# Performance work log

Measured on AMD Instinct MI355X. Metric: run time of the kernel, lower is better.

The kernel has to match this reference:

```python
import jax, jax.numpy as jnp
import numpy as np

H, K, D, HID, B = 8, 2048, 64, 1024, 8192
TEMP = 1.0
LN_EPS = 1e-5


def setup_inputs() -> dict:
    key = jax.random.key(0)
    ks = jax.random.split(key, 6)
    s = lambda k, shape, scale=0.02: jax.random.normal(k, shape, jnp.float32) * scale
    return dict(
        z=jax.random.normal(ks[0], (B, HID), jnp.float32),
        w1=s(ks[1], (H, HID, 2 * D)),
        b1=jnp.zeros((H, 2 * D), jnp.float32),
        w2=s(ks[2], (H, 2 * D, D)),
        b2=jnp.zeros((H, D), jnp.float32),
        ln_g=jnp.ones((H, D), jnp.float32),
        ln_b=jnp.zeros((H, D), jnp.float32),
        codebooks=jax.random.normal(ks[3], (H, K, D), jnp.float32) * 0.1,
        dec_w=s(ks[4], (H, D, HID // H)),
        dec_b=jnp.zeros((H, HID // H), jnp.float32),
    )


def reference(z, w1, b1, w2, b2, ln_g, ln_b, codebooks, dec_w, dec_b):
    sg = jax.lax.stop_gradient
    Bf = z.shape[0]
    # per-head projection MLP (all heads fused via einsum): [B,HID] -> [B,H,2D] -> [B,H,D]
    h1 = jax.nn.gelu(jnp.einsum('bi,hio->bho', z, w1) + b1, approximate=False)
    zh = jnp.einsum('bho,hod->bhd', h1, w2) + b2
    mu = zh.mean(-1, keepdims=True)
    var = zh.var(-1, keepdims=True)  # biased, as torch LayerNorm
    z_heads = (zh - mu) / jnp.sqrt(var + LN_EPS) * ln_g + ln_b  # [B,H,D]
    # squared-distance to codebooks: ||z||^2 + ||c||^2 - 2 z.c  -> [B,H,K]
    z_sq = (z_heads ** 2).sum(-1)[..., None]          # [B,H,1]
    c_sq = (codebooks ** 2).sum(-1)[None]             # [1,H,K]
    zc = jnp.einsum('bhd,hkd->bhk', z_heads, codebooks)
    dists = z_sq + c_sq - 2.0 * zc
    idx = jnp.argmin(dists, axis=-1)                  # [B,H] int
    z_q = codebooks[jnp.arange(H)[None, :], idx]      # gather -> [B,H,D]
    # per-head decoders then concat -> [B,HID]
    dec = lambda x: (jnp.einsum('bhd,hdo->bho', x, dec_w) + dec_b).reshape(Bf, -1)
    z_q_dec = dec(z_q)
    z_proj = dec(z_heads)
    z_q_st = z_proj + sg(z_q_dec - z_proj)
    commit = jnp.mean((z_proj - sg(z_q_dec)) ** 2)
    codebook_loss = jnp.mean((sg(z_proj) - z_q_dec) ** 2)
    # entropy regularizer over soft assignment probs
    probs = jax.nn.softmax(-dists * TEMP, axis=-1)    # [B,H,K]
    avg_probs = probs.mean(0)                         # [H,K]
    entropy = -(avg_probs * jnp.log(avg_probs + 1e-8)).sum(-1).mean()
    entropy_loss = 1.0 - entropy / np.float32(np.log(K))
    # orthogonality: pairwise co-occurrence deviation from independence
    p = jnp.zeros((H, K), jnp.float32).at[jnp.arange(H)[None, :], idx].add(1.0) / Bf  # [H,K]
    ortho = jnp.float32(0.0)
    cnt = 0
    for i in range(H):
        for j in range(i + 1, H):
            co = jnp.zeros((K, K), jnp.float32).at[idx[:, i], idx[:, j]].add(1.0) / (Bf + 1e-8)
            expected = p[i][:, None] * p[j][None, :]
            ortho = ortho + jnp.mean(jnp.abs(co - expected))
            cnt += 1
    ortho = ortho / cnt
    return z_q_st, idx, commit, codebook_loss, entropy_loss, ortho, sg(z_heads)
```

## Files before the change

### kernel.cpp

```cpp
#include <hip/hip_runtime.h>
#include <math.h>

#define H 8
#define KK 2048
#define DD 64
#define HIDN 1024
#define BB 8192
#define TWO_D 128
#define OO 128

#define WS_CSQ   1048576
#define WS_ZSQ   1064960
#define WS_IDX   1130496
#define WS_AVGP  1196032
#define WS_HIST  1212416
#define WS_ACC   1228800
#define WS_ZERO_BYTES ((16384 + 16384 + 4) * 4)

#define OUT_ZQ 0
#define OUT_IDX 8388608
#define OUT_COMMIT 8454144
#define OUT_CBL 8454145
#define OUT_ENT 8454146
#define OUT_ORTHO 8454147
#define OUT_ZH 8454148
#define W2P_OFF 3145728

typedef __attribute__((ext_vector_type(8))) short bf16x8;
typedef __attribute__((ext_vector_type(4))) float f32x4;

__device__ inline unsigned short bf16_rne(float x) {
    union { float f; unsigned u; } c; c.f = x;
    unsigned r = c.u + 0x7FFFu + ((c.u >> 16) & 1u);
    return (unsigned short)(r >> 16);
}
__device__ inline float bf16_f32(unsigned short h) {
    union { unsigned u; float f; } c; c.u = ((unsigned)h) << 16;
    return c.f;
}
__device__ inline void split3(float x, short* hh, short* mm, short* ll) {
    unsigned short h_ = bf16_rne(x);
    float r1 = x - bf16_f32(h_);
    unsigned short m_ = bf16_rne(r1);
    float r2 = r1 - bf16_f32(m_);
    unsigned short l_ = bf16_rne(r2);
    *hh = (short)h_; *mm = (short)m_; *ll = (short)l_;
}

__device__ inline void gload_lds16(const void* g, void* l) {
    __builtin_amdgcn_global_load_lds(
        (const __attribute__((address_space(1))) unsigned int*)g,
        (__attribute__((address_space(3))) unsigned int*)l, 16, 0, 0);
}

__global__ __launch_bounds__(256) void k_pre_w1(const float* __restrict__ w1, float* outp) {
    short* w1p = (short*)outp;
    int h = blockIdx.x >> 5, kc = blockIdx.x & 31;
    int t = threadIdx.x;
    int l = t & 63, w = t >> 6;
    int lb = l & 15, lg = l >> 4;
#pragma unroll
    for (int oi = 0; oi < 2; ++oi) {
        int ot = w + oi * 4;
        union { short e[8]; bf16x8 v; } uh, um, ul;
#pragma unroll
        for (int j = 0; j < 8; ++j) {
            float x = w1[(size_t)(h * HIDN + kc * 32 + lg * 8 + j) * TWO_D + ot * 16 + lb];
            split3(x, &uh.e[j], &um.e[j], &ul.e[j]);
        }
        size_t base = (((size_t)(h * 32 + kc) * 8 + ot) * 3) * 512 + l * 8;
        *(bf16x8*)(w1p + base) = uh.v;
        *(bf16x8*)(w1p + base + 512) = um.v;
        *(bf16x8*)(w1p + base + 1024) = ul.v;
    }
}

__global__ __launch_bounds__(256) void k_pre_w2(const float* __restrict__ w2, float* outp) {
    short* w2p = (short*)outp + W2P_OFF;
    int h = blockIdx.x;
    int t = threadIdx.x;
    int l = t & 63, w = t >> 6;
    int lb = l & 15, lg = l >> 4;
#pragma unroll
    for (int i = 0; i < 4; ++i) {
        int fr = w * 4 + i;
        int dt = fr >> 2, oc = fr & 3;
        union { short e[8]; bf16x8 v; } uh, um, ul;
#pragma unroll
        for (int j = 0; j < 8; ++j) {
            float x = w2[(size_t)(h * TWO_D + oc * 32 + lg * 8 + j) * DD + dt * 16 + lb];
            split3(x, &uh.e[j], &um.e[j], &ul.e[j]);
        }
        size_t base = (((size_t)(h * 4 + dt) * 4 + oc) * 3) * 512 + l * 8;
        *(bf16x8*)(w2p + base) = uh.v;
        *(bf16x8*)(w2p + base + 512) = um.v;
        *(bf16x8*)(w2p + base + 1024) = ul.v;
    }
}

__global__ __launch_bounds__(256) void k_pre(const float* __restrict__ cb, float* __restrict__ ws) {
    int h = blockIdx.x >> 3, kb = blockIdx.x & 7;
    int t = threadIdx.x;
    int l = t & 63;
    int lb = l & 15, lg = l >> 4;
    short* stg = (short*)ws;
#pragma unroll
    for (int p = 0; p < 4; ++p) {
        int T = kb * 16 + p * 4 + (t >> 6);
        int k = T * 16 + lb;
        const float* row = cb + (size_t)(h * KK + k) * DD;
        float4 a0 = *(const float4*)(row + lg * 8);
        float4 a1 = *(const float4*)(row + lg * 8 + 4);
        float4 c0 = *(const float4*)(row + 32 + lg * 8);
        float4 c1 = *(const float4*)(row + 32 + lg * 8 + 4);
        float v0[8] = {a0.x, a0.y, a0.z, a0.w, a1.x, a1.y, a1.z, a1.w};
        float v1[8] = {c0.x, c0.y, c0.z, c0.w, c1.x, c1.y, c1.z, c1.w};
        union { short e[8]; bf16x8 v; } h0, h1;
        float s = 0.f;
#pragma unroll
        for (int j = 0; j < 8; ++j) {
            float x = v0[j];
            s = fmaf(x, x, s);
            h0.e[j] = (short)bf16_rne(x);
            float y = v1[j];
            s = fmaf(y, y, s);
            h1.e[j] = (short)bf16_rne(y);
        }
        size_t base = ((size_t)(h * 128 + T)) * 1024 + l * 8;
        *(bf16x8*)(stg + base) = h0.v;
        *(bf16x8*)(stg + base + 512) = h1.v;
        s += __shfl_xor(s, 16);
        s += __shfl_xor(s, 32);
        if (lg == 0) ws[WS_CSQ + h * KK + k] = s;
    }
}

__global__ __launch_bounds__(512, 4) void k1(const float* __restrict__ z, const float* __restrict__ b1,
                                             const float* __restrict__ b2, const float* __restrict__ lng,
                                             const float* __restrict__ lnb, float* out,
                                             float* __restrict__ ws) {
    __shared__ char SM[51200];
    int t = threadIdx.x;
    int h = blockIdx.y;
    int b0 = blockIdx.x * 64;
    int w = t >> 6, l = t & 63;
    int rg = w >> 1, wc = w & 1;
    int lb = l & 15, lg = l >> 4;

    const short* w2p = (const short*)out + W2P_OFF;
    const char* w1h = (const char*)out + (size_t)h * (32 * 24576);
    const float* zrow = z + (size_t)(b0 + rg * 16 + lb) * HIDN + lg * 8;

    {
        char* lb0 = SM + (t >> 6) * 1024;
        const char* gb = w1h + t * 16;
#pragma unroll
        for (int r = 0; r < 3; ++r) gload_lds16(gb + r * 8192, lb0 + r * 8192);
#pragma unroll
        for (int r = 0; r < 3; ++r) gload_lds16(gb + 24576 + r * 8192, lb0 + 24576 + r * 8192);
    }
    float4 zA = *(const float4*)(zrow);
    float4 zB = *(const float4*)(zrow + 4);
    __syncthreads();

    f32x4 acc[4];
#pragma unroll
    for (int i = 0; i < 4; ++i) acc[i] = (f32x4){0.f, 0.f, 0.f, 0.f};

#pragma unroll
    for (int c = 0; c < 32; ++c) {
        if (c > 0) {
            if (c < 31) asm volatile("s_waitcnt vmcnt(3)" ::: "memory");
            else        asm volatile("s_waitcnt vmcnt(0)" ::: "memory");
            __builtin_amdgcn_sched_barrier(0);
            __builtin_amdgcn_s_barrier();
            __builtin_amdgcn_sched_barrier(0);
        }
        {
            float zc[8] = {zA.x, zA.y, zA.z, zA.w, zB.x, zB.y, zB.z, zB.w};
            union { short e[8]; bf16x8 v; } uh, um, ul;
#pragma unroll
            for (int j = 0; j < 8; ++j) split3(zc[j], &uh.e[j], &um.e[j], &ul.e[j]);
            bf16x8 bh = uh.v, bm = um.v, blo = ul.v;
            const char* bp = SM + (c & 1) * 24576;
#pragma unroll
            for (int ot = 0; ot < 4; ++ot) {
                const char* fb = bp + (wc * 4 + ot) * 3072 + l * 16;
                bf16x8 ah = *(const bf16x8*)(fb);
                bf16x8 am = *(const bf16x8*)(fb + 1024);
                bf16x8 al = *(const bf16x8*)(fb + 2048);
                f32x4 cc = acc[ot];
                cc = __builtin_amdgcn_mfma_f32_16x16x32_bf16(ah, bh, cc, 0, 0, 0);
                cc = __builtin_amdgcn_mfma_f32_16x16x32_bf16(ah, bm, cc, 0, 0, 0);
                cc = __builtin_amdgcn_mfma_f32_16x16x32_bf16(am, bh, cc, 0, 0, 0);
                cc = __builtin_amdgcn_mfma_f32_16x16x32_bf16(ah, blo, cc, 0, 0, 0);
                cc = __builtin_amdgcn_mfma_f32_16x16x32_bf16(al, bh, cc, 0, 0, 0);
                cc = __builtin_amdgcn_mfma_f32_16x16x32_bf16(am, bm, cc, 0, 0, 0);
                acc[ot] = cc;
            }
        }
        __builtin_amdgcn_sched_barrier(0);
        __builtin_amdgcn_s_barrier();
        __builtin_amdgcn_sched_barrier(0);
        if (c < 31) {
            zA = *(const float4*)(zrow + (c + 1) * 32);
            zB = *(const float4*)(zrow + (c + 1) * 32 + 4);
        }
        if (c + 2 < 32) {
            char* lb0 = SM + (c & 1) * 24576 + (t >> 6) * 1024;
            const char* gb = w1h + (size_t)(c + 2) * 24576 + t * 16;
#pragma unroll
            for (int r = 0; r < 3; ++r) gload_lds16(gb + r * 8192, lb0 + r * 8192);
        }
    }
    __syncthreads();

    float* h1L = (float*)SM;
    float* zhL = (float*)(SM + 33792);

#pragma unroll
    for (int ot = 0; ot < 4; ++ot)
#pragma unroll
        for (int r = 0; r < 4; ++r) {
            int o = (wc * 4 + ot) * 16 + lg * 4 + r;
            float x = acc[ot][r] + b1[h * TWO_D + o];
            float gl = 0.5f * x * (1.0f + erff(x * 0.70710678118654752f));
            h1L[(rg * 16 + lb) * 132 + o] = gl;
        }
    __syncthreads();

    f32x4 a2[2];
    a2[0] = (f32x4){0.f, 0.f, 0.f, 0.f};
    a2[1] = (f32x4){0.f, 0.f, 0.f, 0.f};
#pragma unroll
    for (int oc = 0; oc < 4; ++oc) {
        const float* hr = h1L + (rg * 16 + lb) * 132 + oc * 32 + lg * 8;
        union { short e[8]; bf16x8 v; } uh, um, ul;
#pragma unroll
        for (int j = 0; j < 8; ++j) split3(hr[j], &uh.e[j], &um.e[j], &ul.e[j]);
        bf16x8 bh = uh.v, bm = um.v, blo = ul.v;
#pragma unroll
        for (int dti = 0; dti < 2; ++dti) {
            int dt = wc * 2 + dti;
            const short* fb = w2p + (((size_t)(h * 4 + dt) * 4 + oc) * 3) * 512 + l * 8;
            bf16x8 ah = *(const bf16x8*)(fb);
            bf16x8 am = *(const bf16x8*)(fb + 512);
            bf16x8 al = *(const bf16x8*)(fb + 1024);
            f32x4 cc = a2[dti];
            cc = __builtin_amdgcn_mfma_f32_16x16x32_bf16(ah, bh, cc, 0, 0, 0);
            cc = __builtin_amdgcn_mfma_f32_16x16x32_bf16(ah, bm, cc, 0, 0, 0);
            cc = __builtin_amdgcn_mfma_f32_16x16x32_bf16(am, bh, cc, 0, 0, 0);
            cc = __builtin_amdgcn_mfma_f32_16x16x32_bf16(ah, blo, cc, 0, 0, 0);
            cc = __builtin_amdgcn_mfma_f32_16x16x32_bf16(al, bh, cc, 0, 0, 0);
            cc = __builtin_amdgcn_mfma_f32_16x16x32_bf16(am, bm, cc, 0, 0, 0);
            a2[dti] = cc;
        }
    }
#pragma unroll
    for (int dti = 0; dti < 2; ++dti)
#pragma unroll
        for (int r = 0; r < 4; ++r) {
            int d = (wc * 2 + dti) * 16 + lg * 4 + r;
            zhL[(rg * 16 + lb) * 68 + d] = a2[dti][r] + b2[h * DD + d];
        }
    __syncthreads();

    {
        int row = t >> 3, c0 = (t & 7) * 8;
        const float* zr = zhL + row * 68 + c0;
        float v[8];
#pragma unroll
        for (int j = 0; j < 8; ++j) v[j] = zr[j];
        float s = 0.f;
#pragma unroll
        for (int j = 0; j < 8; ++j) s += v[j];
        s += __shfl_xor(s, 1); s += __shfl_xor(s, 2); s += __shfl_xor(s, 4);
        float mu = s * (1.0f / 64.0f);
        float vv = 0.f;
#pragma unroll
        for (int j = 0; j < 8; ++j) { float d = v[j] - mu; vv = fmaf(d, d, vv); }
        vv += __shfl_xor(vv, 1); vv += __shfl_xor(vv, 2); vv += __shfl_xor(vv, 4);
        float rstd = 1.0f / sqrtf(vv * (1.0f / 64.0f) + 1e-5f);
        float zn[8]; float ss = 0.f;
#pragma unroll
        for (int j = 0; j < 8; ++j) {
            float x = (v[j] - mu) * rstd * lng[h * DD + c0 + j] + lnb[h * DD + c0 + j];
            zn[j] = x; ss = fmaf(x, x, ss);
        }
        ss += __shfl_xor(ss, 1); ss += __shfl_xor(ss, 2); ss += __shfl_xor(ss, 4);
        int brow = b0 + row;
        if ((t & 7) == 0) ws[WS_ZSQ + brow * H + h] = ss;
        float4 s0 = {zn[0], zn[1], zn[2], zn[3]};
        float4 s1 = {zn[4], zn[5], zn[6], zn[7]};
        *(float4*)(out + OUT_ZH + (size_t)(brow * H + h) * DD + c0) = s0;
        *(float4*)(out + OUT_ZH + (size_t)(brow * H + h) * DD + c0 + 4) = s1;
    }
}

#define MARGIN 0.10f
__device__ inline void stage16(const char* gsrc, short* lbuf, int t) {
    char* lb_ = (char*)lbuf + (t >> 6) * 1024;
    gload_lds16(gsrc + t * 16, lb_);
}
__global__ __launch_bounds__(1024, 4) void k2(const float* __restrict__ cb,
                                              float* __restrict__ out, float* __restrict__ ws) {
    __shared__ short bufs[3][8192];
    __shared__ float zt[32][68];
    __shared__ float csqL[2048];
    __shared__ float zsqL[32];
    __shared__ float redM[8][32], redS[8][32], redE[8][32];
    __shared__ int   redK[8][32];
    __shared__ float MbL[32], SbL[32];
    __shared__ float paccL[2048];

    int t = threadIdx.x;
    int h = blockIdx.y;
    int b0 = blockIdx.x * 32;
    int w = t >> 6, l = t & 63;
    int rg = w >> 3, kg = w & 7;
    int lb = l & 15, lg = l >> 4;
    int rmy = rg * 16 + lb;

    const char* stgbase = (const char*)ws + (size_t)h * 262144;

    stage16(stgbase, bufs[0], t);
    stage16(stgbase + 16384, bufs[1], t);
    stage16(stgbase + 32768, bufs[2], t);
    for (int i = t; i < 2048; i += 1024) {
        paccL[i] = 0.f;
        csqL[i] = ws[WS_CSQ + h * KK + i];
    }
#pragma unroll
    for (int i = 0; i < 2; ++i) {
        int q = t + i * 1024;
        int r = q >> 6, d = q & 63;
        zt[r][d] = out[OUT_ZH + (size_t)((b0 + r) * H + h) * DD + d];
    }
    if (t < 32) zsqL[t] = ws[WS_ZSQ + (b0 + t) * H + h];
    __syncthreads();

    bf16x8 bh[2], bl[2];
#pragma unroll
    for (int s = 0; s < 2; ++s) {
        const float* zr = &zt[rmy][s * 32 + lg * 8];
        union { short e[8]; bf16x8 v; } uh, ul;
#pragma unroll
        for (int j = 0; j < 8; ++j) {
            float x = zr[j];
            unsigned short hb = bf16_rne(x);
            uh.e[j] = (short)hb;
            ul.e[j] = (short)bf16_rne(x - bf16_f32(hb));
        }
        bh[s] = uh.v; bl[s] = ul.v;
    }

    f32x4 acc[16];
#pragma unroll
    for (int a = 0; a < 16; ++a) acc[a] = (f32x4){0.f, 0.f, 0.f, 0.f};

#pragma unroll
    for (int c = 0; c < 16; ++c) {
        if (c > 0) {
            if (c <= 13)      asm volatile("s_waitcnt vmcnt(2)" ::: "memory");
            else if (c == 14) asm volatile("s_waitcnt vmcnt(1)" ::: "memory");
            else              asm volatile("s_waitcnt vmcnt(0)" ::: "memory");
            __builtin_amdgcn_sched_barrier(0);
            __builtin_amdgcn_s_barrier();
            __builtin_amdgcn_sched_barrier(0);
        }
        {
            const short* fb = bufs[c % 3] + kg * 1024 + l * 8;
            bf16x8 C0 = *(const bf16x8*)(fb);
            bf16x8 C1 = *(const bf16x8*)(fb + 512);
            f32x4 cc = acc[c];
            cc = __builtin_amdgcn_mfma_f32_16x16x32_bf16(bh[0], C0, cc, 0, 0, 0);
            cc = __builtin_amdgcn_mfma_f32_16x16x32_bf16(bl[0], C0, cc, 0, 0, 0);
            cc = __builtin_amdgcn_mfma_f32_16x16x32_bf16(bh[1], C1, cc, 0, 0, 0);
            cc = __builtin_amdgcn_mfma_f32_16x16x32_bf16(bl[1], C1, cc, 0, 0, 0);
            acc[c] = cc;
        }
        if (c < 15) {
            __builtin_amdgcn_sched_barrier(0);
            __builtin_amdgcn_s_barrier();
            __builtin_amdgcn_sched_barrier(0);
            if (c + 3 < 16)
                stage16(stgbase + (size_t)(c + 3) * 16384, bufs[c % 3], t);
        }
    }

    float zsqv[4];
#pragma unroll
    for (int r = 0; r < 4; ++r) zsqv[r] = zsqL[rg * 16 + lg * 4 + r];
    float mn[4] = {3.4e38f, 3.4e38f, 3.4e38f, 3.4e38f};
#pragma unroll
    for (int ai = 0; ai < 16; ++ai) {
        float cs = csqL[(8 * ai + kg) * 16 + lb];
        f32x4 a = acc[ai];
        f32x4 d;
#pragma unroll
        for (int r = 0; r < 4; ++r) {
            float dv = (zsqv[r] + cs) - 2.f * a[r];
            d[r] = dv;
            mn[r] = fminf(mn[r], dv);
        }
        acc[ai] = d;
    }
#pragma unroll
    for (int off = 1; off < 16; off <<= 1)
#pragma unroll
        for (int r = 0; r < 4; ++r) mn[r] = fminf(mn[r], __shfl_xor(mn[r], off));
    if (lb == 0)
#pragma unroll
        for (int r = 0; r < 4; ++r) redM[kg][rg * 16 + lg * 4 + r] = mn[r];
    __syncthreads();
    if (t < 32) {
        float m = redM[0][t];
#pragma unroll
        for (int g = 1; g < 8; ++g) m = fminf(m, redM[g][t]);
        MbL[t] = m;
    }
    __syncthreads();
    float Mb[4];
#pragma unroll
    for (int r = 0; r < 4; ++r) Mb[r] = MbL[rg * 16 + lg * 4 + r];

    float S[4] = {0.f, 0.f, 0.f, 0.f};
    unsigned mk0 = 0, mk1 = 0, mk2 = 0, mk3 = 0;
#pragma unroll
    for (int ai = 0; ai < 16; ++ai) {
        f32x4 d = acc[ai];
        f32x4 e;
#pragma unroll
        for (int r = 0; r < 4; ++r) {
            float dv = d[r];
            float ev = __expf(Mb[r] - dv);
            S[r] += ev;
            e[r] = ev;
            bool cand = dv <= Mb[r] + MARGIN;
            if (r == 0) mk0 |= cand ? (1u << ai) : 0u;
            if (r == 1) mk1 |= cand ? (1u << ai) : 0u;
            if (r == 2) mk2 |= cand ? (1u << ai) : 0u;
            if (r == 3) mk3 |= cand ? (1u << ai) : 0u;
        }
        acc[ai] = e;
    }
#pragma unroll
    for (int off = 1; off < 16; off <<= 1)
#pragma unroll
        for (int r = 0; r < 4; ++r) S[r] += __shfl_xor(S[r], off);
    if (lb == 0)
#pragma unroll
        for (int r = 0; r < 4; ++r) redS[kg][rg * 16 + lg * 4 + r] = S[r];

    float eB[4] = {3.4e38f, 3.4e38f, 3.4e38f, 3.4e38f};
    int kB[4] = {0x7FFFFFFF, 0x7FFFFFFF, 0x7FFFFFFF, 0x7FFFFFFF};
#pragma unroll
    for (int r = 0; r < 4; ++r) {
        unsigned m = (r == 0) ? mk0 : (r == 1) ? mk1 : (r == 2) ? mk2 : mk3;
        const float* zr0 = &zt[rg * 16 + lg * 4 + r][0];
        float eBest = 3.4e38f; int kBest = 0x7FFFFFFF;
        while (m) {
            int ai = (int)__ffs(m) - 1;
            m &= m - 1;
            int k = (8 * ai + kg) * 16 + lb;
            const float4* crow = (const float4*)(cb + (size_t)(h * KK + k) * DD);
            float s = 0.f;
#pragma unroll 1
            for (int q = 0; q < 16; ++q) {
                float4 cv = crow[q];
                s = fmaf(zr0[q * 4 + 0], cv.x, s);
                s = fmaf(zr0[q * 4 + 1], cv.y, s);
                s = fmaf(zr0[q * 4 + 2], cv.z, s);
                s = fmaf(zr0[q * 4 + 3], cv.w, s);
            }
            float ex = (zsqv[r] + csqL[k]) - 2.f * s;
            if (ex < eBest || (ex == eBest && k < kBest)) { eBest = ex; kBest = k; }
        }
        eB[r] = eBest; kB[r] = kBest;
    }
#pragma unroll
    for (int off = 1; off < 16; off <<= 1)
#pragma unroll
        for (int r = 0; r < 4; ++r) {
            float oe = __shfl_xor(eB[r], off);
            int ok = __shfl_xor(kB[r], off);
            if (oe < eB[r] || (oe == eB[r] && ok < kB[r])) { eB[r] = oe; kB[r] = ok; }
        }
    if (lb == 0)
#pragma unroll
        for (int r = 0; r < 4; ++r) {
            redE[kg][rg * 16 + lg * 4 + r] = eB[r];
            redK[kg][rg * 16 + lg * 4 + r] = kB[r];
        }
    __syncthreads();
    if (t < 32) {
        float Sv = redS[0][t];
#pragma unroll
        for (int g = 1; g < 8; ++g) Sv += redS[g][t];
        SbL[t] = Sv;
        float e0 = redE[0][t]; int k0_ = redK[0][t];
#pragma unroll
        for (int g = 1; g < 8; ++g) {
            float oe = redE[g][t]; int ok = redK[g][t];
            if (oe < e0 || (oe == e0 && ok < k0_)) { e0 = oe; k0_ = ok; }
        }
        out[OUT_IDX + (b0 + t) * H + h] = (float)k0_;
        ((int*)ws)[WS_IDX + (b0 + t) * H + h] = k0_;
        atomicAdd(((unsigned*)ws) + WS_HIST + h * KK + k0_, 1u);
    }
    __syncthreads();
    float invS[4];
#pragma unroll
    for (int r = 0; r < 4; ++r) invS[r] = 1.0f / SbL[rg * 16 + lg * 4 + r];

#pragma unroll
    for (int ai = 0; ai < 16; ++ai) {
        f32x4 e = acc[ai];
        float v = e[0] * invS[0];
        v = fmaf(e[1], invS[1], v);
        v = fmaf(e[2], invS[2], v);
        v = fmaf(e[3], invS[3], v);
        v += __shfl_xor(v, 16);
        v += __shfl_xor(v, 32);
        if (lg == 0) atomicAdd(&paccL[(8 * ai + kg) * 16 + lb], v);
    }
    __syncthreads();
    for (int i = t; i < 2048; i += 1024)
        atomicAdd(ws + WS_AVGP + h * KK + i, paccL[i]);
}

__global__ __launch_bounds__(256, 2) void k3(const float* __restrict__ cb, const float* __restrict__ dw,
                                             const float* __restrict__ db, float* __restrict__ out,
                                             float* __restrict__ ws) {
    __shared__ float zqt[32][65];
    __shared__ float zht[32][65];
    __shared__ float dwt[64][128];
    __shared__ int idxs[32];
    __shared__ double redc[4];
    int t = threadIdx.x;
    int h = blockIdx.y;
    int b0 = blockIdx.x * 32;
    if (t < 32) idxs[t] = ((const int*)ws)[WS_IDX + (b0 + t) * H + h];
    __syncthreads();
#pragma unroll
    for (int p = 0; p < 8; ++p) {
        int q = t + 256 * p;
        int r = q >> 6, d = q & 63;
        zqt[r][d] = cb[(size_t)(h * KK + idxs[r]) * DD + d];
        zht[r][d] = out[OUT_ZH + (size_t)((b0 + r) * H + h) * DD + d];
    }
#pragma unroll
    for (int p = 0; p < 8; ++p) {
        int q = t + 256 * p;
        int r = q >> 5, c4 = q & 31;
        *(float4*)(&dwt[r][c4 * 4]) = *(const float4*)(dw + (size_t)(h * DD + r) * OO + c4 * 4);
    }
    __syncthreads();
    int rg = t >> 4, cg = t & 15;
    float aq[2][8], ap[2][8];
#pragma unroll
    for (int i = 0; i < 2; ++i)
#pragma unroll
        for (int j = 0; j < 8; ++j) { aq[i][j] = 0.f; ap[i][j] = 0.f; }
#pragma unroll 4
    for (int d = 0; d < 64; ++d) {
        float q0 = zqt[rg * 2][d], q1 = zqt[rg * 2 + 1][d];
        float p0 = zht[rg * 2][d], p1 = zht[rg * 2 + 1][d];
        float4 wa = *(const float4*)(&dwt[d][cg * 8]);
        float4 wb = *(const float4*)(&dwt[d][cg * 8 + 4]);
        float ww[8] = {wa.x, wa.y, wa.z, wa.w, wb.x, wb.y, wb.z, wb.w};
#pragma unroll
        for (int j = 0; j < 8; ++j) {
            aq[0][j] = fmaf(q0, ww[j], aq[0][j]);
            aq[1][j] = fmaf(q1, ww[j], aq[1][j]);
            ap[0][j] = fmaf(p0, ww[j], ap[0][j]);
            ap[1][j] = fmaf(p1, ww[j], ap[1][j]);
        }
    }
    float lsum = 0.f;
#pragma unroll
    for (int i = 0; i < 2; ++i) {
        float vq4[8];
#pragma unroll
        for (int j = 0; j < 8; ++j) {
            float bb = db[h * OO + cg * 8 + j];
            float vq = aq[i][j] + bb;
            float vp = ap[i][j] + bb;
            vq4[j] = vp + (vq - vp);
            float e = vp - vq;
            lsum = fmaf(e, e, lsum);
        }
        float4 s0 = {vq4[0], vq4[1], vq4[2], vq4[3]};
        float4 s1 = {vq4[4], vq4[5], vq4[6], vq4[7]};
        size_t o = (size_t)(b0 + rg * 2 + i) * HIDN + h * OO + cg * 8;
        *(float4*)(out + OUT_ZQ + o) = s0;
        *(float4*)(out + OUT_ZQ + o + 4) = s1;
    }
#pragma unroll
    for (int off = 1; off < 64; off <<= 1) lsum += __shfl_xor(lsum, off);
    if ((t & 63) == 0) redc[t >> 6] = (double)lsum;
    __syncthreads();
    if (t == 0) atomicAdd((double*)(ws + WS_ACC), redc[0] + redc[1] + redc[2] + redc[3]);
}

__global__ __launch_bounds__(256) void k6(float* __restrict__ ws) {
    __shared__ unsigned slots[16384];
    __shared__ unsigned cnts[16384];
    int t = threadIdx.x;
    int bid = blockIdx.x;
    int pi = 0, pj = 1;
    {
        int c = 0;
        for (int a = 0; a < H; ++a)
            for (int b = a + 1; b < H; ++b) { if (c == bid) { pi = a; pj = b; } ++c; }
    }
    for (int s = t; s < 16384; s += 256) { slots[s] = 0xFFFFFFFFu; cnts[s] = 0u; }
    __syncthreads();
    const int* idxi = ((const int*)ws) + WS_IDX;
    for (int b = t; b < BB; b += 256) {
        unsigned key = ((unsigned)idxi[b * H + pi] << 11) | (unsigned)idxi[b * H + pj];
        unsigned p = (key * 2654435761u) >> 18;
        while (true) {
            unsigned old = atomicCAS(&slots[p], 0xFFFFFFFFu, key);
            if (old == 0xFFFFFFFFu || old == key) { atomicAdd(&cnts[p], 1u); break; }
            p = (p + 1) & 16383u;
        }
    }
    __syncthreads();
    const unsigned* hist = ((const unsigned*)ws) + WS_HIST;
    double loc = 0.0;
    for (int s = t; s < 16384; s += 256) {
        unsigned key = slots[s];
        if (key != 0xFFFFFFFFu) {
            int ki = (int)(key >> 11), kj = (int)(key & 2047u);
            float c = (float)cnts[s] * (1.0f / 8192.0f);
            float piv = (float)hist[pi * KK + ki] * (1.0f / 8192.0f);
            float pjv = (float)hist[pj * KK + kj] * (1.0f / 8192.0f);
            float e = piv * pjv;
            loc += (double)fabsf(c - e) - (double)e;
        }
    }
    double spi = 0.0, spj = 0.0;
    for (int k = t; k < KK; k += 256) {
        spi += (double)hist[pi * KK + k];
        spj += (double)hist[pj * KK + k];
    }
#pragma unroll
    for (int off = 1; off < 64; off <<= 1) {
        loc += __shfl_xor(loc, off);
        spi += __shfl_xor(spi, off);
        spj += __shfl_xor(spj, off);
    }
    __syncthreads();
    double* sc = (double*)cnts;
    if ((t & 63) == 0) { int w = t >> 6; sc[w] = loc; sc[4 + w] = spi; sc[8 + w] = spj; }
    __syncthreads();
    if (t == 0) {
        double L = sc[0] + sc[1] + sc[2] + sc[3];
        double SPI = (sc[4] + sc[5] + sc[6] + sc[7]) / 8192.0;
        double SPJ = (sc[8] + sc[9] + sc[10] + sc[11]) / 8192.0;
        atomicAdd(((double*)(ws + WS_ACC)) + 1, L + SPI * SPJ);
    }
}

__global__ __launch_bounds__(256) void k4(float* __restrict__ out, float* __restrict__ ws) {
    __shared__ double red[256];
    int t = threadIdx.x;
    double tot = 0.0;
    for (int h = 0; h < H; ++h) {
        double s = 0.0;
        for (int k = t; k < KK; k += 256) {
            double a = (double)ws[WS_AVGP + h * KK + k] / 8192.0;
            s += a * log(a + 1e-8);
        }
        tot += s;
    }
    red[t] = tot;
    __syncthreads();
    for (int off = 128; off; off >>= 1) {
        if (t < off) red[t] += red[t + off];
        __syncthreads();
    }
    if (t == 0) {
        double entropy = -red[0] / 8.0;
        out[OUT_ENT] = (float)(1.0 - entropy / log(2048.0));
        double ca = *(const double*)(ws + WS_ACC);
        float cm = (float)(ca / (8192.0 * 1024.0));
        out[OUT_COMMIT] = cm;
        out[OUT_CBL] = cm;
        double oa = *(((const double*)(ws + WS_ACC)) + 1);
        out[OUT_ORTHO] = (float)(oa / (28.0 * 4194304.0));
    }
}

extern "C" void kernel_launch(void* const* d_in, const int* in_sizes, int n_in,
                              void* d_out, int out_size, void* d_ws, size_t ws_size,
                              hipStream_t stream) {
    (void)in_sizes; (void)n_in; (void)out_size; (void)ws_size;
    const float* z   = (const float*)d_in[0];
    const float* w1  = (const float*)d_in[1];
    const float* b1  = (const float*)d_in[2];
    const float* w2  = (const float*)d_in[3];
    const float* b2  = (const float*)d_in[4];
    const float* lng = (const float*)d_in[5];
    const float* lnb = (const float*)d_in[6];
    const float* cb  = (const float*)d_in[7];
    const float* dw  = (const float*)d_in[8];
    const float* db  = (const float*)d_in[9];
    float* out = (float*)d_out;
    float* ws = (float*)d_ws;

    hipMemsetAsync(ws + WS_AVGP, 0, WS_ZERO_BYTES, stream);
    k_pre_w1<<<256, 256, 0, stream>>>(w1, out);
    k_pre_w2<<<8, 256, 0, stream>>>(w2, out);
    k_pre<<<64, 256, 0, stream>>>(cb, ws);
    k1<<<dim3(128, 8), 512, 0, stream>>>(z, b1, b2, lng, lnb, out, ws);
    k2<<<dim3(256, 8), 1024, 0, stream>>>(cb, out, ws);
    k3<<<dim3(256, 8), 256, 0, stream>>>(cb, dw, db, out, ws);
    k6<<<28, 256, 0, stream>>>(ws);
    k4<<<1, 256, 0, stream>>>(out, ws);
}
```

Baseline: 537.4 us.

## Double k1 row tile per block, remap codebook staging, drop k2 LDS csq/pacc buffers

k1 now processes 128 batch rows per block, with each wave owning 16 full rows and all 8 output tiles, so each staged w1 tile in LDS is reused across twice as many rows. The second GEMM is split into two halves to fit the per-wave h1 scratch in LDS. The codebook staging order in k_pre is permuted so each k2 wave group reads a contiguous codebook range, which lets k2 drop its LDS copies of c_sq and the avg-prob accumulator and use direct global loads and global atomics instead. The trade-offs are more registers and LDS in k1, fewer k1 blocks, and more global atomic traffic in k2.

```diff
diff --git a/kernel.cpp b/kernel.cpp
--- a/kernel.cpp
+++ b/kernel.cpp
@@ -101,8 +101,7 @@
 __global__ __launch_bounds__(256) void k_pre(const float* __restrict__ cb, float* __restrict__ ws) {
     int h = blockIdx.x >> 3, kb = blockIdx.x & 7;
     int t = threadIdx.x;
-    int l = t & 63;
-    int lb = l & 15, lg = l >> 4;
+    int lb = t & 15, lg = (t >> 4) & 3;
     short* stg = (short*)ws;
 #pragma unroll
     for (int p = 0; p < 4; ++p) {
@@ -126,7 +125,8 @@
             s = fmaf(y, y, s);
             h1.e[j] = (short)bf16_rne(y);
         }
-        size_t base = ((size_t)(h * 128 + T)) * 1024 + l * 8;
+        int off = (T & 15) * 8 + (T >> 4);
+        size_t base = ((size_t)(h * 128 + off)) * 1024 + (t & 63) * 8;
         *(bf16x8*)(stg + base) = h0.v;
         *(bf16x8*)(stg + base + 512) = h1.v;
         s += __shfl_xor(s, 16);
@@ -139,17 +139,16 @@
                                              const float* __restrict__ b2, const float* __restrict__ lng,
                                              const float* __restrict__ lnb, float* out,
                                              float* __restrict__ ws) {
-    __shared__ char SM[51200];
+    __shared__ char SM[69632];
     int t = threadIdx.x;
     int h = blockIdx.y;
-    int b0 = blockIdx.x * 64;
+    int b0 = blockIdx.x * 128;
     int w = t >> 6, l = t & 63;
-    int rg = w >> 1, wc = w & 1;
     int lb = l & 15, lg = l >> 4;
 
     const short* w2p = (const short*)out + W2P_OFF;
     const char* w1h = (const char*)out + (size_t)h * (32 * 24576);
-    const float* zrow = z + (size_t)(b0 + rg * 16 + lb) * HIDN + lg * 8;
+    const float* zrow = z + (size_t)(b0 + w * 16 + lb) * HIDN + lg * 8;
 
     {
         char* lb0 = SM + (t >> 6) * 1024;
@@ -163,9 +162,9 @@
     float4 zB = *(const float4*)(zrow + 4);
     __syncthreads();
 
-    f32x4 acc[4];
-#pragma unroll
-    for (int i = 0; i < 4; ++i) acc[i] = (f32x4){0.f, 0.f, 0.f, 0.f};
+    f32x4 acc[8];
+#pragma unroll
+    for (int i = 0; i < 8; ++i) acc[i] = (f32x4){0.f, 0.f, 0.f, 0.f};
 
 #pragma unroll
     for (int c = 0; c < 32; ++c) {
@@ -184,8 +183,8 @@
             bf16x8 bh = uh.v, bm = um.v, blo = ul.v;
             const char* bp = SM + (c & 1) * 24576;
 #pragma unroll
-            for (int ot = 0; ot < 4; ++ot) {
-                const char* fb = bp + (wc * 4 + ot) * 3072 + l * 16;
+            for (int ot = 0; ot < 8; ++ot) {
+                const char* fb = bp + ot * 3072 + l * 16;
                 bf16x8 ah = *(const bf16x8*)(fb);
                 bf16x8 am = *(const bf16x8*)(fb + 1024);
                 bf16x8 al = *(const bf16x8*)(fb + 2048);
@@ -215,103 +214,110 @@
     }
     __syncthreads();
 
-    float* h1L = (float*)SM;
-    float* zhL = (float*)(SM + 33792);
-
-#pragma unroll
-    for (int ot = 0; ot < 4; ++ot)
+    float* h1W = (float*)SM + w * (16 * 68);
+    float* zhL = (float*)(SM + 34816);
+
+    f32x4 a2[4];
+#pragma unroll
+    for (int i = 0; i < 4; ++i) a2[i] = (f32x4){0.f, 0.f, 0.f, 0.f};
+
+#pragma unroll
+    for (int half = 0; half < 2; ++half) {
+#pragma unroll
+        for (int oti = 0; oti < 4; ++oti) {
+            int ot = half * 4 + oti;
+#pragma unroll
+            for (int r = 0; r < 4; ++r) {
+                int o = ot * 16 + lg * 4 + r;
+                float x = acc[ot][r] + b1[h * TWO_D + o];
+                float gl = 0.5f * x * (1.0f + erff(x * 0.70710678118654752f));
+                h1W[lb * 68 + (o - half * 64)] = gl;
+            }
+        }
+        __syncthreads();
+#pragma unroll
+        for (int oci = 0; oci < 2; ++oci) {
+            int oc = half * 2 + oci;
+            const float* hr = h1W + lb * 68 + oci * 32 + lg * 8;
+            union { short e[8]; bf16x8 v; } uh, um, ul;
+#pragma unroll
+            for (int j = 0; j < 8; ++j) split3(hr[j], &uh.e[j], &um.e[j], &ul.e[j]);
+            bf16x8 bh = uh.v, bm = um.v, blo = ul.v;
+#pragma unroll
+            for (int dt = 0; dt < 4; ++dt) {
+                const short* fb = w2p + (((size_t)(h * 4 + dt) * 4 + oc) * 3) * 512 + l * 8;
+                bf16x8 ah = *(const bf16x8*)(fb);
+                bf16x8 am = *(const bf16x8*)(fb + 512);
+                bf16x8 al = *(const bf16x8*)(fb + 1024);
+                f32x4 cc = a2[dt];
+                cc = __builtin_amdgcn_mfma_f32_16x16x32_bf16(ah, bh, cc, 0, 0, 0);
+                cc = __builtin_amdgcn_mfma_f32_16x16x32_bf16(ah, bm, cc, 0, 0, 0);
+                cc = __builtin_amdgcn_mfma_f32_16x16x32_bf16(am, bh, cc, 0, 0, 0);
+                cc = __builtin_amdgcn_mfma_f32_16x16x32_bf16(ah, blo, cc, 0, 0, 0);
+                cc = __builtin_amdgcn_mfma_f32_16x16x32_bf16(al, bh, cc, 0, 0, 0);
+                cc = __builtin_amdgcn_mfma_f32_16x16x32_bf16(am, bm, cc, 0, 0, 0);
+                a2[dt] = cc;
+            }
+        }
+        __syncthreads();
+    }
+
+#pragma unroll
+    for (int dt = 0; dt < 4; ++dt)
 #pragma unroll
         for (int r = 0; r < 4; ++r) {
-            int o = (wc * 4 + ot) * 16 + lg * 4 + r;
-            float x = acc[ot][r] + b1[h * TWO_D + o];
-            float gl = 0.5f * x * (1.0f + erff(x * 0.70710678118654752f));
-            h1L[(rg * 16 + lb) * 132 + o] = gl;
-        }
-    __syncthreads();
-
-    f32x4 a2[2];
-    a2[0] = (f32x4){0.f, 0.f, 0.f, 0.f};
-    a2[1] = (f32x4){0.f, 0.f, 0.f, 0.f};
-#pragma unroll
-    for (int oc = 0; oc < 4; ++oc) {
-        const float* hr = h1L + (rg * 16 + lb) * 132 + oc * 32 + lg * 8;
-        union { short e[8]; bf16x8 v; } uh, um, ul;
-#pragma unroll
-        for (int j = 0; j < 8; ++j) split3(hr[j], &uh.e[j], &um.e[j], &ul.e[j]);
-        bf16x8 bh = uh.v, bm = um.v, blo = ul.v;
-#pragma unroll
-        for (int dti = 0; dti < 2; ++dti) {
-            int dt = wc * 2 + dti;
-            const short* fb = w2p + (((size_t)(h * 4 + dt) * 4 + oc) * 3) * 512 + l * 8;
-            bf16x8 ah = *(const bf16x8*)(fb);
-            bf16x8 am = *(const bf16x8*)(fb + 512);
-            bf16x8 al = *(const bf16x8*)(fb + 1024);
-            f32x4 cc = a2[dti];
-            cc = __builtin_amdgcn_mfma_f32_16x16x32_bf16(ah, bh, cc, 0, 0, 0);
-            cc = __builtin_amdgcn_mfma_f32_16x16x32_bf16(ah, bm, cc, 0, 0, 0);
-            cc = __builtin_amdgcn_mfma_f32_16x16x32_bf16(am, bh, cc, 0, 0, 0);
-            cc = __builtin_amdgcn_mfma_f32_16x16x32_bf16(ah, blo, cc, 0, 0, 0);
-            cc = __builtin_amdgcn_mfma_f32_16x16x32_bf16(al, bh, cc, 0, 0, 0);
-            cc = __builtin_amdgcn_mfma_f32_16x16x32_bf16(am, bm, cc, 0, 0, 0);
-            a2[dti] = cc;
-        }
-    }
-#pragma unroll
-    for (int dti = 0; dti < 2; ++dti)
-#pragma unroll
-        for (int r = 0; r < 4; ++r) {
-            int d = (wc * 2 + dti) * 16 + lg * 4 + r;
-            zhL[(rg * 16 + lb) * 68 + d] = a2[dti][r] + b2[h * DD + d];
+            int d = dt * 16 + lg * 4 + r;
+            zhL[(w * 16 + lb) * 68 + d] = a2[dt][r] + b2[h * DD + d];
         }
     __syncthreads();
 
     {
-        int row = t >> 3, c0 = (t & 7) * 8;
+        int row = t >> 2, c0 = (t & 3) * 16;
         const float* zr = zhL + row * 68 + c0;
-        float v[8];
-#pragma unroll
-        for (int j = 0; j < 8; ++j) v[j] = zr[j];
+        float v[16];
+#pragma unroll
+        for (int j = 0; j < 16; ++j) v[j] = zr[j];
         float s = 0.f;
 #pragma unroll
-        for (int j = 0; j < 8; ++j) s += v[j];
-        s += __shfl_xor(s, 1); s += __shfl_xor(s, 2); s += __shfl_xor(s, 4);
+        for (int j = 0; j < 16; ++j) s += v[j];
+        s += __shfl_xor(s, 1); s += __shfl_xor(s, 2);
         float mu = s * (1.0f / 64.0f);
         float vv = 0.f;
 #pragma unroll
-        for (int j = 0; j < 8; ++j) { float d = v[j] - mu; vv = fmaf(d, d, vv); }
-        vv += __shfl_xor(vv, 1); vv += __shfl_xor(vv, 2); vv += __shfl_xor(vv, 4);
+        for (int j = 0; j < 16; ++j) { float d = v[j] - mu; vv = fmaf(d, d, vv); }
+        vv += __shfl_xor(vv, 1); vv += __shfl_xor(vv, 2);
         float rstd = 1.0f / sqrtf(vv * (1.0f / 64.0f) + 1e-5f);
-        float zn[8]; float ss = 0.f;
-#pragma unroll
-        for (int j = 0; j < 8; ++j) {
+        float zn[16]; float ss = 0.f;
+#pragma unroll
+        for (int j = 0; j < 16; ++j) {
             float x = (v[j] - mu) * rstd * lng[h * DD + c0 + j] + lnb[h * DD + c0 + j];
             zn[j] = x; ss = fmaf(x, x, ss);
         }
-        ss += __shfl_xor(ss, 1); ss += __shfl_xor(ss, 2); ss += __shfl_xor(ss, 4);
+        ss += __shfl_xor(ss, 1); ss += __shfl_xor(ss, 2);
         int brow = b0 + row;
-        if ((t & 7) == 0) ws[WS_ZSQ + brow * H + h] = ss;
-        float4 s0 = {zn[0], zn[1], zn[2], zn[3]};
-        float4 s1 = {zn[4], zn[5], zn[6], zn[7]};
-        *(float4*)(out + OUT_ZH + (size_t)(brow * H + h) * DD + c0) = s0;
-        *(float4*)(out + OUT_ZH + (size_t)(brow * H + h) * DD + c0 + 4) = s1;
+        if ((t & 3) == 0) ws[WS_ZSQ + brow * H + h] = ss;
+#pragma unroll
+        for (int q = 0; q < 4; ++q) {
+            float4 sv = {zn[q * 4 + 0], zn[q * 4 + 1], zn[q * 4 + 2], zn[q * 4 + 3]};
+            *(float4*)(out + OUT_ZH + (size_t)(brow * H + h) * DD + c0 + q * 4) = sv;
+        }
     }
 }
 
 #define MARGIN 0.10f
-__device__ inline void stage16(const char* gsrc, short* lbuf, int t) {
+__device__ inline void stage16k(const char* gsrc, short* lbuf, int t) {
     char* lb_ = (char*)lbuf + (t >> 6) * 1024;
-    gload_lds16(gsrc + t * 16, lb_);
-}
-__global__ __launch_bounds__(1024, 4) void k2(const float* __restrict__ cb,
-                                              float* __restrict__ out, float* __restrict__ ws) {
+    const char* gb = gsrc + t * 16;
+    gload_lds16(gb, lb_);
+}
+__global__ __launch_bounds__(1024) void k2(const float* __restrict__ cb,
+                                           float* __restrict__ out, float* __restrict__ ws) {
     __shared__ short bufs[3][8192];
     __shared__ float zt[32][68];
-    __shared__ float csqL[2048];
-    __shared__ float zsqL[32];
     __shared__ float redM[8][32], redS[8][32], redE[8][32];
     __shared__ int   redK[8][32];
     __shared__ float MbL[32], SbL[32];
-    __shared__ float paccL[2048];
+    __shared__ float zsqL[32];
 
     int t = threadIdx.x;
     int h = blockIdx.y;
@@ -323,13 +329,9 @@
 
     const char* stgbase = (const char*)ws + (size_t)h * 262144;
 
-    stage16(stgbase, bufs[0], t);
-    stage16(stgbase + 16384, bufs[1], t);
-    stage16(stgbase + 32768, bufs[2], t);
-    for (int i = t; i < 2048; i += 1024) {
-        paccL[i] = 0.f;
-        csqL[i] = ws[WS_CSQ + h * KK + i];
-    }
+    stage16k(stgbase, bufs[0], t);
+    stage16k(stgbase + 16384, bufs[1], t);
+    stage16k(stgbase + 32768, bufs[2], t);
 #pragma unroll
     for (int i = 0; i < 2; ++i) {
         int q = t + i * 1024;
@@ -339,7 +341,7 @@
     if (t < 32) zsqL[t] = ws[WS_ZSQ + (b0 + t) * H + h];
     __syncthreads();
 
-    bf16x8 bh[2], bl[2];
+    bf16x8 bh[2], blo[2];
 #pragma unroll
     for (int s = 0; s < 2; ++s) {
         const float* zr = &zt[rmy][s * 32 + lg * 8];
@@ -351,7 +353,7 @@
             uh.e[j] = (short)hb;
             ul.e[j] = (short)bf16_rne(x - bf16_f32(hb));
         }
-        bh[s] = uh.v; bl[s] = ul.v;
+        bh[s] = uh.v; blo[s] = ul.v;
     }
 
     f32x4 acc[16];
@@ -374,9 +376,9 @@
             bf16x8 C1 = *(const bf16x8*)(fb + 512);
             f32x4 cc = acc[c];
             cc = __builtin_amdgcn_mfma_f32_16x16x32_bf16(bh[0], C0, cc, 0, 0, 0);
-            cc = __builtin_amdgcn_mfma_f32_16x16x32_bf16(bl[0], C0, cc, 0, 0, 0);
+            cc = __builtin_amdgcn_mfma_f32_16x16x32_bf16(blo[0], C0, cc, 0, 0, 0);
             cc = __builtin_amdgcn_mfma_f32_16x16x32_bf16(bh[1], C1, cc, 0, 0, 0);
-            cc = __builtin_amdgcn_mfma_f32_16x16x32_bf16(bl[1], C1, cc, 0, 0, 0);
+            cc = __builtin_amdgcn_mfma_f32_16x16x32_bf16(blo[1], C1, cc, 0, 0, 0);
             acc[c] = cc;
         }
         if (c < 15) {
@@ -384,7 +386,7 @@
             __builtin_amdgcn_s_barrier();
             __builtin_amdgcn_sched_barrier(0);
             if (c + 3 < 16)
-                stage16(stgbase + (size_t)(c + 3) * 16384, bufs[c % 3], t);
+                stage16k(stgbase + (size_t)(c + 3) * 16384, bufs[c % 3], t);
         }
     }
 
@@ -394,7 +396,7 @@
     float mn[4] = {3.4e38f, 3.4e38f, 3.4e38f, 3.4e38f};
 #pragma unroll
     for (int ai = 0; ai < 16; ++ai) {
-        float cs = csqL[(8 * ai + kg) * 16 + lb];
+        float cs = ws[WS_CSQ + h * KK + kg * 256 + ai * 16 + lb];
         f32x4 a = acc[ai];
         f32x4 d;
 #pragma unroll
@@ -462,7 +464,7 @@
         while (m) {
             int ai = (int)__ffs(m) - 1;
             m &= m - 1;
-            int k = (8 * ai + kg) * 16 + lb;
+            int k = kg * 256 + ai * 16 + lb;
             const float4* crow = (const float4*)(cb + (size_t)(h * KK + k) * DD);
             float s = 0.f;
 #pragma unroll 1
@@ -473,7 +475,7 @@
                 s = fmaf(zr0[q * 4 + 2], cv.z, s);
                 s = fmaf(zr0[q * 4 + 3], cv.w, s);
             }
-            float ex = (zsqv[r] + csqL[k]) - 2.f * s;
+            float ex = (zsqv[r] + ws[WS_CSQ + h * KK + k]) - 2.f * s;
             if (ex < eBest || (ex == eBest && k < kBest)) { eBest = ex; kBest = k; }
         }
         eB[r] = eBest; kB[r] = kBest;
@@ -522,11 +524,8 @@
         v = fmaf(e[3], invS[3], v);
         v += __shfl_xor(v, 16);
         v += __shfl_xor(v, 32);
-        if (lg == 0) atomicAdd(&paccL[(8 * ai + kg) * 16 + lb], v);
-    }
-    __syncthreads();
-    for (int i = t; i < 2048; i += 1024)
-        atomicAdd(ws + WS_AVGP + h * KK + i, paccL[i]);
+        if (lg == 0) atomicAdd(ws + WS_AVGP + h * KK + kg * 256 + ai * 16 + lb, v);
+    }
 }
 
 __global__ __launch_bounds__(256, 2) void k3(const float* __restrict__ cb, const float* __restrict__ dw,
@@ -714,7 +713,7 @@
     k_pre_w1<<<256, 256, 0, stream>>>(w1, out);
     k_pre_w2<<<8, 256, 0, stream>>>(w2, out);
     k_pre<<<64, 256, 0, stream>>>(cb, ws);
-    k1<<<dim3(128, 8), 512, 0, stream>>>(z, b1, b2, lng, lnb, out, ws);
+    k1<<<dim3(64, 8), 512, 0, stream>>>(z, b1, b2, lng, lnb, out, ws);
     k2<<<dim3(256, 8), 1024, 0, stream>>>(cb, out, ws);
     k3<<<dim3(256, 8), 256, 0, stream>>>(cb, dw, db, out, ws);
     k6<<<28, 256, 0, stream>>>(ws);
```

After: 515.2 us. -4.1%, faster.
